# Kernel tuning notes

Hardware: AMD Instinct MI355X
Metric: run time of the kernel (lower is better)

Reference implementation:

```python
import jax, jax.numpy as jnp
import numpy as np
from jax import lax

DIM = 512
DH = 16          # dim_head
H = DIM // DH    # 32 heads
WS = 7           # window_size
SR = 3           # sr_ratio (AvgPool2d kernel, stride=1)
EPS = 1e-5


def _rel_pos_indices():
    # mirrors the torch buffer construction, incl. the [:, 24:] slice for sr_ratio>1
    pos = np.arange(WS)
    gi, gj = np.meshgrid(pos, pos, indexing='ij')
    grid = np.stack([gi, gj], axis=-1).reshape(-1, 2)            # (49, 2)
    rel = grid[:, None, :] - grid[None, :, :] + (WS - 1)         # (49, 49, 2)
    idx = rel[..., 0] * (2 * WS - 1) + rel[..., 1]               # (49, 49)
    return jnp.asarray(idx[:, 24:], dtype=jnp.int32)             # (49, 25)


def _layernorm(x, g, b):
    m = jnp.mean(x, axis=-1, keepdims=True)
    v = jnp.mean(jnp.square(x - m), axis=-1, keepdims=True)
    return (x - m) * lax.rsqrt(v + EPS) * g + b


def setup_inputs() -> dict:
    key = jax.random.key(0)
    ks = jax.random.split(key, 8)
    B, X, Y = 8, 14, 14
    x = jax.random.normal(ks[0], (B, X, Y, WS, WS, DIM), dtype=jnp.float32)
    ln_gamma = 1.0 + 0.1 * jax.random.normal(ks[1], (DIM,), dtype=jnp.float32)
    ln_beta = 0.1 * jax.random.normal(ks[2], (DIM,), dtype=jnp.float32)
    s = 1.0 / np.sqrt(DIM)
    Wq = jax.random.normal(ks[3], (DIM, DIM), dtype=jnp.float32) * s
    Wkv = jax.random.normal(ks[4], (2 * DIM, DIM), dtype=jnp.float32) * s
    Wout = jax.random.normal(ks[5], (DIM, DIM), dtype=jnp.float32) * s
    rel_pos_emb = 0.02 * jax.random.normal(ks[6], ((2 * WS - 1) ** 2, H), dtype=jnp.float32)
    return {"x": x, "ln_gamma": ln_gamma, "ln_beta": ln_beta,
            "Wq": Wq, "Wkv": Wkv, "Wout": Wout, "rel_pos_emb": rel_pos_emb}


def reference(x, ln_gamma, ln_beta, Wq, Wkv, Wout, rel_pos_emb):
    B, X, Y, W1, W2, D = x.shape
    Nw = B * X * Y                      # number of windows
    Nq = W1 * W2                        # 49 query tokens per window
    xn = _layernorm(x, ln_gamma, ln_beta)
    xw = xn.reshape(Nw, Nq, D)
    # queries
    q = (xw @ Wq.T).reshape(Nw, Nq, H, DH).transpose(0, 2, 1, 3) * (DH ** -0.5)  # (Nw,H,Nq,DH)
    # KV spatial reduction: AvgPool2d(kernel=SR, stride=1) over the 7x7 window
    xi = xw.reshape(Nw, W1, W2, D)
    xp = lax.reduce_window(xi, 0.0, lax.add, (1, SR, SR, 1), (1, 1, 1, 1), 'VALID') / (SR * SR)
    Hp, Wp = W1 - SR + 1, W2 - SR + 1   # 5, 5
    xkv = _layernorm(xp.reshape(Nw, Hp * Wp, D), ln_gamma, ln_beta)
    # to_kv with einops '(dim h l)' decomposition: last axis factored as (DH, H, 2)
    kv = (xkv @ Wkv.T).reshape(Nw, Hp * Wp, DH, H, 2)
    k = kv[..., 0].transpose(0, 3, 1, 2)  # (Nw, H, Nk, DH)
    v = kv[..., 1].transpose(0, 3, 1, 2)
    sim = jnp.einsum('bhid,bhjd->bhij', q, k)                    # (Nw,H,49,25)
    bias = rel_pos_emb[_rel_pos_indices()]                       # (49,25,H)
    sim = sim + bias.transpose(2, 0, 1)[None]
    attn = jax.nn.softmax(sim, axis=-1)
    out = jnp.einsum('bhij,bhjd->bhid', attn, v)                 # (Nw,H,49,DH)
    out = out.reshape(Nw, H, W1, W2, DH).transpose(0, 2, 3, 1, 4).reshape(Nw, W1, W2, D)
    out = out @ Wout.T
    return out.reshape(B, X, Y, W1, W2, D)
```

## Files before the change

kernel.cpp:

```cpp
#include <hip/hip_runtime.h>

typedef _Float16 half8 __attribute__((ext_vector_type(8)));
typedef float f32x4 __attribute__((ext_vector_type(4)));

#define MFMA16(a,b,c) __builtin_amdgcn_mfma_f32_16x16x32_f16(a,b,c,0,0,0)
#define GLOAD16(g, l) __builtin_amdgcn_global_load_lds( \
  (const __attribute__((address_space(1))) void*)(g), \
  (__attribute__((address_space(3))) void*)(l), 16, 0, 0)

static constexpr int NW     = 1568;
static constexpr int MROWSQ = 76832;
static constexpr int MPADQ  = 76928;
static constexpr int MROWKV = 39200;
static constexpr int MPADKV = 39296;
static constexpr float LOG2E = 1.4426950408889634f;

__device__ __forceinline__ half8 h8z(){
  half8 z = {(_Float16)0,(_Float16)0,(_Float16)0,(_Float16)0,
             (_Float16)0,(_Float16)0,(_Float16)0,(_Float16)0};
  return z;
}

__global__ void k_prep_w(const float* __restrict__ a, const float* __restrict__ b,
                         const float* __restrict__ c,
                         _Float16* __restrict__ ah, _Float16* __restrict__ bh,
                         _Float16* __restrict__ ch){
  int i = blockIdx.x*256 + threadIdx.x;
  if(i < 262144) ah[i] = (_Float16)(a[i]*(0.25f*LOG2E));
  int j = i - 262144;
  if(j >= 0 && j < 524288) bh[j] = (_Float16)b[j];
  int k = i - 786432;
  if(k >= 0 && k < 262144) ch[k] = (_Float16)c[k];
}

__global__ void k_prep_bias(const float* __restrict__ rel, float* __restrict__ biasT){
  int t = blockIdx.x*256 + threadIdx.x;
  if(t >= 65536) return;
  int h = t >> 11;
  int r = t & 2047;
  int i = r >> 5, slotk = r & 31;
  int kg = slotk >> 3, idx = slotk & 7;
  int j = (idx < 4) ? (kg*4 + idx) : (16 + kg*4 + idx - 4);
  float v = 0.f;
  if(j >= 25) v = -1e30f;
  else if(i < 49){
    int qi = i/7, qj = i%7;
    int c = j + 24, ki = c/7, kj = c%7;
    v = rel[((qi-ki+6)*13 + (qj-kj+6))*32 + h];
  }
  biasT[t] = v*LOG2E;
}

__global__ __launch_bounds__(512) void k_ln_pool(const float* __restrict__ x,
    const float* __restrict__ gamma, const float* __restrict__ beta,
    _Float16* __restrict__ xn, _Float16* __restrict__ xkv){
  __shared__ _Float16 nrm[49*512];
  const int w = blockIdx.x, t = threadIdx.x;
  const int lane = t & 63, wv = t >> 6;
  float gf[8], bf[8];
  {
    float4 g0 = *(const float4*)(gamma + lane*8);
    float4 g1 = *(const float4*)(gamma + lane*8 + 4);
    float4 b0 = *(const float4*)(beta  + lane*8);
    float4 b1 = *(const float4*)(beta  + lane*8 + 4);
    gf[0]=g0.x; gf[1]=g0.y; gf[2]=g0.z; gf[3]=g0.w;
    gf[4]=g1.x; gf[5]=g1.y; gf[6]=g1.z; gf[7]=g1.w;
    bf[0]=b0.x; bf[1]=b0.y; bf[2]=b0.z; bf[3]=b0.w;
    bf[4]=b1.x; bf[5]=b1.y; bf[6]=b1.z; bf[7]=b1.w;
  }
  const float* xw = x + (size_t)w*49*512;
  for(int i = wv; i < 49; i += 8){
    const float* row = xw + i*512 + lane*8;
    float4 v0 = *(const float4*)row;
    float4 v1 = *(const float4*)(row+4);
    float v[8] = {v0.x,v0.y,v0.z,v0.w,v1.x,v1.y,v1.z,v1.w};
    float s = 0.f, sq = 0.f;
    #pragma unroll
    for(int j=0;j<8;j++){ s += v[j]; sq += v[j]*v[j]; }
    #pragma unroll
    for(int o=32;o>=1;o>>=1){ s += __shfl_xor(s,o); sq += __shfl_xor(sq,o); }
    float mean = s*(1.f/512.f);
    float rstd = rsqrtf(sq*(1.f/512.f) - mean*mean + 1e-5f);
    half8 nh;
    #pragma unroll
    for(int j=0;j<8;j++)
      nh[j] = (_Float16)((v[j]-mean)*rstd*gf[j] + bf[j]);
    *(half8*)&nrm[i*512 + lane*8] = nh;
    *(half8*)(xn + ((size_t)w*49 + i)*512 + lane*8) = nh;
  }
  __syncthreads();
  for(int p = wv; p < 25; p += 8){
    const int pi = p/5, pj = p%5;
    float acc[8] = {0,0,0,0,0,0,0,0};
    #pragma unroll
    for(int a=0;a<3;a++)
      #pragma unroll
      for(int bb=0;bb<3;bb++){
        half8 rv = *(const half8*)&nrm[((pi+a)*7 + (pj+bb))*512 + lane*8];
        #pragma unroll
        for(int j=0;j<8;j++) acc[j] += (float)rv[j];
      }
    float s = 0.f, sq = 0.f;
    #pragma unroll
    for(int j=0;j<8;j++){ acc[j] *= (1.f/9.f); s += acc[j]; sq += acc[j]*acc[j]; }
    #pragma unroll
    for(int o=32;o>=1;o>>=1){ s += __shfl_xor(s,o); sq += __shfl_xor(sq,o); }
    float mean = s*(1.f/512.f);
    float rstd = rsqrtf(sq*(1.f/512.f) - mean*mean + 1e-5f);
    half8 nh;
    #pragma unroll
    for(int j=0;j<8;j++) nh[j] = (_Float16)((acc[j]-mean)*rstd*gf[j] + bf[j]);
    *(half8*)(xkv + ((size_t)w*25 + p)*512 + lane*8) = nh;
  }
}

template<int MODE>
__global__ __launch_bounds__(256) void k_gemm(const _Float16* __restrict__ A,
    const _Float16* __restrict__ Bw, _Float16* __restrict__ oh,
    float* __restrict__ of, int ldc, int ntn, int nwg){
  __shared__ __align__(16) _Float16 As[2][128*32];
  __shared__ __align__(16) _Float16 Bs[2][128*32];
  const int orig = blockIdx.x;
  const int xcd = orig & 7, slot = orig >> 3;
  const int q8 = nwg >> 3, r8 = nwg & 7;
  const int base = (xcd < r8) ? xcd*(q8+1) : r8*(q8+1) + (xcd-r8)*q8;
  const int lin = base + slot;
  const int m0 = (lin / ntn) * 128, n0 = (lin % ntn) * 128;
  const int t = threadIdx.x, lane = t & 63;
  const int wid = t >> 6, wm = (wid>>1)*64, wn = (wid&1)*64;
  const int lr = lane & 15, kg = lane >> 4;
  const _Float16* Ab = A  + (size_t)m0*512;
  const _Float16* Bb = Bw + (size_t)n0*512;
  const int foff0 = wid*64, foff1 = 256 + wid*64;
  const int f0 = foff0 + lane, f1 = foff1 + lane;
  const int r0 = f0 >> 2, r1 = f1 >> 2;
  const size_t ga0 = (size_t)r0*512 + ((f0&3) ^ ((r0>>1)&3))*8;
  const size_t ga1 = (size_t)r1*512 + ((f1&3) ^ ((r1>>1)&3))*8;
  const int swz = (lr>>1) & 3;

  GLOAD16(Ab + ga0, &As[0][foff0*8]);
  GLOAD16(Bb + ga0, &Bs[0][foff0*8]);
  GLOAD16(Ab + ga1, &As[0][foff1*8]);
  GLOAD16(Bb + ga1, &Bs[0][foff1*8]);
  __syncthreads();

  f32x4 acc[4][4] = {};
  int cur = 0;
  for(int kt = 0; kt < 16; ++kt){
    if(kt < 15){
      const int k0 = (kt+1)*32;
      GLOAD16(Ab + ga0 + k0, &As[cur^1][foff0*8]);
      GLOAD16(Bb + ga0 + k0, &Bs[cur^1][foff0*8]);
      GLOAD16(Ab + ga1 + k0, &As[cur^1][foff1*8]);
      GLOAD16(Bb + ga1 + k0, &Bs[cur^1][foff1*8]);
    }
    half8 af[4], bf[4];
    #pragma unroll
    for(int mt=0;mt<4;mt++)
      af[mt] = *(const half8*)&As[cur][(wm + mt*16 + lr)*32 + (kg ^ swz)*8];
    #pragma unroll
    for(int nt=0;nt<4;nt++)
      bf[nt] = *(const half8*)&Bs[cur][(wn + nt*16 + lr)*32 + (kg ^ swz)*8];
    #pragma unroll
    for(int mt=0;mt<4;mt++)
      #pragma unroll
      for(int nt=0;nt<4;nt++)
        acc[mt][nt] = MFMA16(af[mt], bf[nt], acc[mt][nt]);
    __syncthreads();
    cur ^= 1;
  }
  #pragma unroll
  for(int mt=0;mt<4;mt++)
    #pragma unroll
    for(int nt=0;nt<4;nt++)
      #pragma unroll
      for(int r=0;r<4;r++){
        int row = m0 + wm + mt*16 + kg*4 + r;
        int col = n0 + wn + nt*16 + lr;
        float vv = acc[mt][nt][r];
        if(MODE == 0){
          oh[(size_t)row*ldc + col] = (_Float16)vv;
        } else {
          if(row < MROWSQ) of[(size_t)row*ldc + col] = vv;
        }
      }
}

__global__ __launch_bounds__(256) void k_repack(const _Float16* __restrict__ kvb,
    _Float16* __restrict__ kb, _Float16* __restrict__ vb){
  __shared__ uint2 s2[6400];
  uint32_t* su = (uint32_t*)s2;
  const int w = blockIdx.x, t = threadIdx.x;
  const uint2* src = (const uint2*)(kvb + (size_t)w*25*1024);
  #pragma unroll
  for(int it=0; it<25; ++it){
    int U = it*256 + t;
    int j = U >> 8, u = U & 255;
    s2[j*256 + (u ^ (u>>4) ^ (j&15))] = src[U];
  }
  __syncthreads();
  _Float16* kdst = kb + (size_t)w*12800;
  _Float16* vdst = vb + (size_t)w*12800;
  for(int it=0; it<7; ++it){
    int q = it*256 + t;
    if(q < 1600){
      int h = q/50, rem = q%50, j = rem>>1, half = rem&1;
      half8 k8, v8;
      #pragma unroll
      for(int jj=0;jj<8;jj++){
        int dh = half*8 + jj;
        int slot = j*256 + ((dh*16 + (h>>1)) ^ dh ^ (j&15));
        uint32_t val = su[slot*2 + (h&1)];
        k8[jj] = ((_Float16*)&val)[0];
        v8[jj] = ((_Float16*)&val)[1];
      }
      *(half8*)(kdst + q*8) = k8;
      *(half8*)(vdst + q*8) = v8;
    }
  }
}

__global__ __launch_bounds__(256) void k_attn(const _Float16* __restrict__ q,
    const _Float16* __restrict__ kb, const _Float16* __restrict__ vb,
    const float* __restrict__ biasT, _Float16* __restrict__ ao){
  const int w = blockIdx.x, hi = blockIdx.y, t = threadIdx.x;
  const int lane = t & 63, wv = t >> 6;
  const int lr = lane & 15, kg = lane >> 4;
  const size_t qbase = ((size_t)w*49)*512;
  const int hA = hi*4 + wv;
  const size_t kvA = (((size_t)w*32 + hA)*25)*16;
  const size_t kvB = kvA + 6400;
  half8 kA0=h8z(), kA1=h8z(), kB0=h8z(), kB1=h8z();
  if(kg < 2){
    kA0 = *(const half8*)(kb + kvA + lr*16 + kg*8);
    kB0 = *(const half8*)(kb + kvB + lr*16 + kg*8);
    if(lr < 9){
      kA1 = *(const half8*)(kb + kvA + (16+lr)*16 + kg*8);
      kB1 = *(const half8*)(kb + kvB + (16+lr)*16 + kg*8);
    }
  }
  half8 qA[4], qB[4];
  #pragma unroll
  for(int qt=0;qt<4;qt++){
    if(kg < 2){
      const _Float16* p = q + qbase + (size_t)(qt*16+lr)*512 + hA*16 + kg*8;
      qA[qt] = *(const half8*)p;
      qB[qt] = *(const half8*)(p + 256);
    } else { qA[qt] = h8z(); qB[qt] = h8z(); }
  }
  half8 vA = h8z(), vB = h8z();
  #pragma unroll
  for(int idx=0; idx<8; idx++){
    int key = (idx<4) ? (kg*4+idx) : (16 + kg*4 + idx-4);
    if(key < 25){
      vA[idx] = vb[kvA + key*16 + lr];
      vB[idx] = vb[kvB + key*16 + lr];
    }
  }
  const float4* btA = (const float4*)(biasT + (size_t)hA*2048);
  const float4* btB = (const float4*)(biasT + (size_t)(hA+16)*2048);
  #pragma unroll
  for(int qt=0;qt<4;qt++){
    f32x4 sA0={}, sA1={}, sB0={}, sB1={};
    sA0 = MFMA16(kA0, qA[qt], sA0);
    sA1 = MFMA16(kA1, qA[qt], sA1);
    sB0 = MFMA16(kB0, qB[qt], sB0);
    sB1 = MFMA16(kB1, qB[qt], sB1);
    const int i = qt*16 + lr;
    const int bidx = i*8 + kg*2;
    float4 bA0 = btA[bidx], bA1 = btA[bidx+1];
    float4 bB0 = btB[bidx], bB1 = btB[bidx+1];
    float a[8], b[8];
    a[0]=sA0[0]+bA0.x; a[1]=sA0[1]+bA0.y; a[2]=sA0[2]+bA0.z; a[3]=sA0[3]+bA0.w;
    a[4]=sA1[0]+bA1.x; a[5]=sA1[1]+bA1.y; a[6]=sA1[2]+bA1.z; a[7]=sA1[3]+bA1.w;
    b[0]=sB0[0]+bB0.x; b[1]=sB0[1]+bB0.y; b[2]=sB0[2]+bB0.z; b[3]=sB0[3]+bB0.w;
    b[4]=sB1[0]+bB1.x; b[5]=sB1[1]+bB1.y; b[6]=sB1[2]+bB1.z; b[7]=sB1[3]+bB1.w;
    float mA = a[0], mB = b[0];
    #pragma unroll
    for(int j=1;j<8;j++){ mA = fmaxf(mA, a[j]); mB = fmaxf(mB, b[j]); }
    mA = fmaxf(mA, __shfl_xor(mA,16)); mB = fmaxf(mB, __shfl_xor(mB,16));
    mA = fmaxf(mA, __shfl_xor(mA,32)); mB = fmaxf(mB, __shfl_xor(mB,32));
    float sumA = 0.f, sumB = 0.f;
    #pragma unroll
    for(int j=0;j<8;j++){
      a[j] = exp2f(a[j]-mA); sumA += a[j];
      b[j] = exp2f(b[j]-mB); sumB += b[j];
    }
    sumA += __shfl_xor(sumA,16); sumB += __shfl_xor(sumB,16);
    sumA += __shfl_xor(sumA,32); sumB += __shfl_xor(sumB,32);
    float invA = 1.f/sumA, invB = 1.f/sumB;
    half8 pA, pB;
    #pragma unroll
    for(int j=0;j<8;j++){
      pA[j] = (_Float16)(a[j]*invA);
      pB[j] = (_Float16)(b[j]*invB);
    }
    f32x4 oA={}, oB={};
    oA = MFMA16(pA, vA, oA);
    oB = MFMA16(pB, vB, oB);
    #pragma unroll
    for(int r=0;r<4;r++){
      int qi2 = qt*16 + kg*4 + r;
      if(qi2 < 49){
        _Float16* dst = ao + qbase + (size_t)qi2*512 + hA*16 + lr;
        dst[0]   = (_Float16)oA[r];
        dst[256] = (_Float16)oB[r];
      }
    }
  }
}

extern "C" void kernel_launch(void* const* d_in, const int* in_sizes, int n_in,
                              void* d_out, int out_size, void* d_ws, size_t ws_size,
                              hipStream_t stream){
  (void)in_sizes; (void)n_in; (void)out_size; (void)ws_size;
  const float* x    = (const float*)d_in[0];
  const float* gam  = (const float*)d_in[1];
  const float* bet  = (const float*)d_in[2];
  const float* Wq   = (const float*)d_in[3];
  const float* Wkv  = (const float*)d_in[4];
  const float* Wout = (const float*)d_in[5];
  const float* rel  = (const float*)d_in[6];
  float* out = (float*)d_out;

  char* ws = (char*)d_ws;
  size_t off = 0;
  auto alloc = [&](size_t n){ char* p = ws + off; off += (n + 1023) & ~(size_t)1023; return p; };
  _Float16* xn    = (_Float16*)alloc((size_t)MPADQ*512*2);
  _Float16* xkv   = (_Float16*)alloc((size_t)MPADKV*512*2);
  _Float16* kvb   = (_Float16*)alloc((size_t)MPADKV*1024*2);
  _Float16* kbuf  = (_Float16*)alloc((size_t)NW*32*25*16*2);
  _Float16* vbuf  = (_Float16*)alloc((size_t)NW*32*25*16*2);
  _Float16* wqh   = (_Float16*)alloc((size_t)262144*2);
  _Float16* wkvh  = (_Float16*)alloc((size_t)524288*2);
  _Float16* wouth = (_Float16*)alloc((size_t)262144*2);
  float*    biasT = (float*)   alloc((size_t)65536*4);
  _Float16* qb    = kvb;

  k_prep_w   <<<dim3(4096), 256, 0, stream>>>(Wq, Wkv, Wout, wqh, wkvh, wouth);
  k_prep_bias<<<dim3(256),  256, 0, stream>>>(rel, biasT);
  k_ln_pool  <<<dim3(NW),   512, 0, stream>>>(x, gam, bet, xn, xkv);
  k_gemm<0>  <<<dim3(2456), 256, 0, stream>>>(xkv, wkvh, kvb, nullptr, 1024, 8, 2456);
  k_repack   <<<dim3(NW),   256, 0, stream>>>(kvb, kbuf, vbuf);
  k_gemm<0>  <<<dim3(2404), 256, 0, stream>>>(xn,  wqh,  qb,  nullptr,  512, 4, 2404);
  k_attn     <<<dim3(NW,4), 256, 0, stream>>>(qb, kbuf, vbuf, biasT, xn);
  k_gemm<1>  <<<dim3(2404), 256, 0, stream>>>(xn,  wouth, nullptr, out, 512, 4, 2404);
}
```

Baseline: 396.2 us.

## Triple-buffer GEMM LDS tiles with explicit vmcnt waits for deeper prefetch

The GEMM main loop moves from a double-buffered LDS pipeline with full __syncthreads to a three-stage ring buffer that prefetches two K-tiles ahead. It uses explicit s_waitcnt vmcnt counts so each iteration waits only for the tile it is about to consume, plus raw s_barrier calls fenced by sched_barrier. The aim is to hide more global-load latency behind MFMA work. In exchange, LDS use rises from 32KB to 48KB per block, which may lower occupancy, and the hand-counted vmcnt values must match the number of outstanding loads exactly.

Result: faster. 386.7 us (-2.4%).

```diff
diff --git a/kernel.cpp b/kernel.cpp
--- a/kernel.cpp
+++ b/kernel.cpp
@@ -7,6 +7,7 @@
 #define GLOAD16(g, l) __builtin_amdgcn_global_load_lds( \
   (const __attribute__((address_space(1))) void*)(g), \
   (__attribute__((address_space(3))) void*)(l), 16, 0, 0)
+#define SCHEDB() __builtin_amdgcn_sched_barrier(0)
 
 static constexpr int NW     = 1568;
 static constexpr int MROWSQ = 76832;
@@ -118,8 +119,8 @@
 __global__ __launch_bounds__(256) void k_gemm(const _Float16* __restrict__ A,
     const _Float16* __restrict__ Bw, _Float16* __restrict__ oh,
     float* __restrict__ of, int ldc, int ntn, int nwg){
-  __shared__ __align__(16) _Float16 As[2][128*32];
-  __shared__ __align__(16) _Float16 Bs[2][128*32];
+  __shared__ __align__(16) _Float16 As[3][128*32];
+  __shared__ __align__(16) _Float16 Bs[3][128*32];
   const int orig = blockIdx.x;
   const int xcd = orig & 7, slot = orig >> 3;
   const int q8 = nwg >> 3, r8 = nwg & 7;
@@ -138,36 +139,47 @@
   const size_t ga1 = (size_t)r1*512 + ((f1&3) ^ ((r1>>1)&3))*8;
   const int swz = (lr>>1) & 3;
 
-  GLOAD16(Ab + ga0, &As[0][foff0*8]);
-  GLOAD16(Bb + ga0, &Bs[0][foff0*8]);
-  GLOAD16(Ab + ga1, &As[0][foff1*8]);
-  GLOAD16(Bb + ga1, &Bs[0][foff1*8]);
-  __syncthreads();
+  auto STAGE = [&](int buf, int kt){
+    const int k0 = kt*32;
+    GLOAD16(Ab + ga0 + k0, &As[buf][foff0*8]);
+    GLOAD16(Bb + ga0 + k0, &Bs[buf][foff0*8]);
+    GLOAD16(Ab + ga1 + k0, &As[buf][foff1*8]);
+    GLOAD16(Bb + ga1 + k0, &Bs[buf][foff1*8]);
+  };
+  STAGE(0, 0);
+  STAGE(1, 1);
 
   f32x4 acc[4][4] = {};
-  int cur = 0;
+  int buf = 0;
   for(int kt = 0; kt < 16; ++kt){
-    if(kt < 15){
-      const int k0 = (kt+1)*32;
-      GLOAD16(Ab + ga0 + k0, &As[cur^1][foff0*8]);
-      GLOAD16(Bb + ga0 + k0, &Bs[cur^1][foff0*8]);
-      GLOAD16(Ab + ga1 + k0, &As[cur^1][foff1*8]);
-      GLOAD16(Bb + ga1 + k0, &Bs[cur^1][foff1*8]);
-    }
+    if(kt + 2 < 16){
+      int nb = buf + 2; if(nb >= 3) nb -= 3;
+      STAGE(nb, kt + 2);
+    }
+    if(kt < 14)       asm volatile("s_waitcnt vmcnt(8)" ::: "memory");
+    else if(kt == 14) asm volatile("s_waitcnt vmcnt(4)" ::: "memory");
+    else              asm volatile("s_waitcnt vmcnt(0)" ::: "memory");
+    SCHEDB();
+    __builtin_amdgcn_s_barrier();
+    SCHEDB();
+    const _Float16* Ac = As[buf];
+    const _Float16* Bc = Bs[buf];
     half8 af[4], bf[4];
     #pragma unroll
     for(int mt=0;mt<4;mt++)
-      af[mt] = *(const half8*)&As[cur][(wm + mt*16 + lr)*32 + (kg ^ swz)*8];
+      af[mt] = *(const half8*)&Ac[(wm + mt*16 + lr)*32 + (kg ^ swz)*8];
     #pragma unroll
     for(int nt=0;nt<4;nt++)
-      bf[nt] = *(const half8*)&Bs[cur][(wn + nt*16 + lr)*32 + (kg ^ swz)*8];
+      bf[nt] = *(const half8*)&Bc[(wn + nt*16 + lr)*32 + (kg ^ swz)*8];
     #pragma unroll
     for(int mt=0;mt<4;mt++)
       #pragma unroll
       for(int nt=0;nt<4;nt++)
         acc[mt][nt] = MFMA16(af[mt], bf[nt], acc[mt][nt]);
-    __syncthreads();
-    cur ^= 1;
+    SCHEDB();
+    __builtin_amdgcn_s_barrier();
+    SCHEDB();
+    buf += 1; if(buf >= 3) buf -= 3;
   }
   #pragma unroll
   for(int mt=0;mt<4;mt++)
```
